# Performance work log

Hardware: AMD Instinct MI355X
Metric: run time of the kernel (lower is better)

Reference implementation:

```python
import jax, jax.numpy as jnp
import numpy as np

NUM_HOPS = 3

def _position_encoding(sentence_size, embedding_size):
    # Vectorized version of the double loop in the source.
    i = np.arange(1, embedding_size + 1, dtype=np.float32)[:, None]  # [E,1]
    j = np.arange(1, sentence_size + 1, dtype=np.float32)[None, :]   # [1,S]
    enc = (i - embedding_size / 2.0) * (j - sentence_size / 2.0)
    enc = 1.0 + 4.0 * enc / embedding_size / sentence_size
    return jnp.asarray(np.transpose(enc))  # [S, E]

def setup_inputs() -> dict:
    key = jax.random.key(0)
    ks = jax.random.split(key, 9)
    B, M, S, E, V, OUT = 16, 512, 32, 128, 32000, 128
    scale = 0.02
    return {
        "queries": jax.random.randint(ks[0], (B, S), 0, V, dtype=jnp.int32),
        "stories": jax.random.randint(ks[1], (B, M, S), 0, V, dtype=jnp.int32),
        "query_biases": jax.random.normal(ks[2], (V - 1, E), jnp.float32) * scale,
        "stories_biases": jax.random.normal(ks[3], (V - 1, E), jnp.float32) * scale,
        "memory_biases": jax.random.normal(ks[4], (M, E), jnp.float32) * scale,
        "output_biases": jax.random.normal(ks[5], (V - 1, E), jnp.float32) * scale,
        "w_intermediate": jax.random.normal(ks[6], (E, E), jnp.float32) * scale,
        "w_output": jax.random.normal(ks[7], (E, OUT), jnp.float32) * scale,
        "w_final": jax.random.normal(ks[8], (OUT, V), jnp.float32) * scale,
    }

def reference(queries, stories, query_biases, stories_biases, memory_biases,
              output_biases, w_intermediate, w_output, w_final):
    B, M, S = stories.shape
    E = query_biases.shape[1]
    enc = _position_encoding(S, E)  # [S, E]
    nil = jnp.zeros((1, E), dtype=query_biases.dtype)

    # Story memory: gather -> positional weight -> reduce over sentence axis.
    st_tab = jnp.concatenate([stories_biases, nil], axis=0)          # [V, E]
    mem_emb = st_tab[stories]                                        # [B,M,S,E]
    memory = jnp.einsum('bmse,se->bme', mem_emb, enc) + memory_biases

    # Query embedding.
    q_tab = jnp.concatenate([query_biases, nil], axis=0)
    q = jnp.einsum('bse,se->be', q_tab[queries], enc)                # [B,E]

    # Output memory.
    o_tab = jnp.concatenate([output_biases, nil], axis=0)
    output = jnp.einsum('bmse,se->bme', o_tab[stories], enc)         # [B,M,E]

    out_layer = q
    for hop in range(NUM_HOPS):
        probs = jax.nn.softmax(jnp.einsum('bme,be->bm', memory, q))  # [B,M]
        layer_out = jnp.einsum('bme,bm->be', output, probs)          # [B,E]
        w = w_output if hop == NUM_HOPS - 1 else w_intermediate
        out_layer = (q + layer_out) @ w
        q = out_layer                     # pre-nonlinearity state, as in source
        out_layer = jax.nn.relu(out_layer)

    return out_layer @ w_final            # [B, vocab]
```

## Files before the change

kernel.cpp:

```cpp
#include <hip/hip_runtime.h>

constexpr int kB  = 16;
constexpr int kM  = 512;
constexpr int kS  = 32;
constexpr int kE  = 128;
constexpr int kV  = 32000;
constexpr int kVN = kV - 1;
constexpr int kMS = 132;

__global__ __launch_bounds__(256) void embed_stories_kernel(
    const int*   __restrict__ stories,
    const float* __restrict__ st_bias,
    const float* __restrict__ out_bias,
    const float* __restrict__ mem_bias,
    float*       __restrict__ memory,
    float*       __restrict__ output,
    unsigned*    __restrict__ bar)
{
    __shared__ int sidx[2][kS];
    __shared__ __align__(16) float pm[8][kE];
    __shared__ __align__(16) float po[8][kE];

    const int t    = threadIdx.x;
    const int row0 = blockIdx.x * 2;
    if (t < 64) sidx[t >> 5][t & 31] = stories[row0 * kS + t];
    if (blockIdx.x == 0 && t < kB) bar[t] = 0u;
    __syncthreads();

    const int g    = t >> 5;
    const int lane = t & 31;
    const int p    = g >> 2;
    const int ph   = g & 3;
    const int e0   = lane * 4;
    const float ef0 = (float)(e0 - 63), ef1 = (float)(e0 - 62);
    const float ef2 = (float)(e0 - 61), ef3 = (float)(e0 - 60);

    float4 am = {0.f, 0.f, 0.f, 0.f};
    float4 ao = {0.f, 0.f, 0.f, 0.f};
    #pragma unroll
    for (int j = 0; j < 8; ++j) {
        const int s   = ph * 8 + j;
        const int idx = sidx[p][s];
        const int ci  = idx < kVN ? idx : (kVN - 1);
        const float live = (idx < kVN) ? 1.0f : 0.0f;
        const float sf = (float)(s - 15) * (1.0f / 1024.0f);
        const float4 vm = *(const float4*)(st_bias  + (size_t)ci * kE + e0);
        const float4 vo = *(const float4*)(out_bias + (size_t)ci * kE + e0);
        const float c0 = fmaf(ef0, sf, 1.0f) * live;
        const float c1 = fmaf(ef1, sf, 1.0f) * live;
        const float c2 = fmaf(ef2, sf, 1.0f) * live;
        const float c3 = fmaf(ef3, sf, 1.0f) * live;
        am.x = fmaf(vm.x, c0, am.x); am.y = fmaf(vm.y, c1, am.y);
        am.z = fmaf(vm.z, c2, am.z); am.w = fmaf(vm.w, c3, am.w);
        ao.x = fmaf(vo.x, c0, ao.x); ao.y = fmaf(vo.y, c1, ao.y);
        ao.z = fmaf(vo.z, c2, ao.z); ao.w = fmaf(vo.w, c3, ao.w);
    }
    *(float4*)&pm[g][e0] = am;
    *(float4*)&po[g][e0] = ao;
    __syncthreads();

    const int pr = t >> 7;
    const int e  = t & 127;
    const int row = row0 + pr;
    const int m   = row & (kM - 1);
    const float sm = pm[pr * 4 + 0][e] + pm[pr * 4 + 1][e] +
                     pm[pr * 4 + 2][e] + pm[pr * 4 + 3][e];
    const float so = po[pr * 4 + 0][e] + po[pr * 4 + 1][e] +
                     po[pr * 4 + 2][e] + po[pr * 4 + 3][e];
    memory[(size_t)row * kE + e] = sm + mem_bias[m * kE + e];
    output[(size_t)row * kE + e] = so;
}

__device__ __forceinline__ void group_barrier(unsigned* ctr, unsigned target)
{
    __syncthreads();
    if (threadIdx.x == 0) {
        __hip_atomic_fetch_add(ctr, 1u, __ATOMIC_RELEASE, __HIP_MEMORY_SCOPE_AGENT);
        while (__hip_atomic_load(ctr, __ATOMIC_RELAXED, __HIP_MEMORY_SCOPE_AGENT) < target)
            __builtin_amdgcn_s_sleep(2);
    }
    __syncthreads();
}
__device__ __forceinline__ void cstore(float* p, float v) {
    __hip_atomic_store(p, v, __ATOMIC_RELAXED, __HIP_MEMORY_SCOPE_AGENT);
}
__device__ __forceinline__ float cload(const float* p) {
    return __hip_atomic_load(p, __ATOMIC_RELAXED, __HIP_MEMORY_SCOPE_AGENT);
}

__global__ __launch_bounds__(1024) void hops_kernel(
    const int*   __restrict__ queries,
    const float* __restrict__ q_bias,
    const float* __restrict__ memory,
    const float* __restrict__ output,
    const float* __restrict__ w_int,
    const float* __restrict__ w_out,
    float*       __restrict__ numer,
    float*       __restrict__ denom,
    float*       __restrict__ xg,
    unsigned*    __restrict__ bar)
{
    __shared__ __align__(16) float mem_lds[128 * kMS];
    __shared__ __align__(16) float out_lds[128 * kE];
    __shared__ float sc_q[128];
    __shared__ __align__(16) float q_s[kE];
    __shared__ float xb[kE];
    __shared__ __align__(16) float part8[8][kE];
    __shared__ int qidx[kS];

    const int bid = blockIdx.x;
    const int b   = bid >> 2;
    const int qtr = bid & 3;
    const int t   = threadIdx.x;
    unsigned* ctr = bar + b;

    const float* memb = memory + ((size_t)b * kM + qtr * 128) * kE;
    const float* outb = output + ((size_t)b * kM + qtr * 128) * kE;
    #pragma unroll
    for (int i = 0; i < 4; ++i) {
        const int flat = t + i * 1024;
        const int rr = flat >> 5, ff = (flat & 31) * 4;
        *(float4*)&mem_lds[rr * kMS + ff] = *(const float4*)&memb[(size_t)rr * kE + ff];
        *(float4*)&out_lds[rr * kE  + ff] = *(const float4*)&outb[(size_t)rr * kE + ff];
    }
    if (t < kS) qidx[t] = queries[b * kS + t];
    __syncthreads();

    if (t < 256) {
        const int g = t >> 5, lane = t & 31, e0 = lane * 4;
        const float f0 = (float)(e0 - 63) * (1.0f / 1024.0f);
        const float f1 = (float)(e0 - 62) * (1.0f / 1024.0f);
        const float f2 = (float)(e0 - 61) * (1.0f / 1024.0f);
        const float f3 = (float)(e0 - 60) * (1.0f / 1024.0f);
        float4 a = {0.f, 0.f, 0.f, 0.f};
        #pragma unroll
        for (int j = 0; j < 4; ++j) {
            const int s   = g * 4 + j;
            const int idx = qidx[s];
            const int ci  = idx < kVN ? idx : (kVN - 1);
            const float live = (idx < kVN) ? 1.0f : 0.0f;
            const float sf = (float)(s - 15);
            const float4 v = *(const float4*)&q_bias[(size_t)ci * kE + e0];
            a.x = fmaf(v.x, fmaf(f0, sf, 1.f) * live, a.x);
            a.y = fmaf(v.y, fmaf(f1, sf, 1.f) * live, a.y);
            a.z = fmaf(v.z, fmaf(f2, sf, 1.f) * live, a.z);
            a.w = fmaf(v.w, fmaf(f3, sf, 1.f) * live, a.w);
        }
        *(float4*)&part8[g][e0] = a;
    }
    __syncthreads();
    if (t < kE) {
        float s = 0.f;
        #pragma unroll
        for (int g = 0; g < 8; ++g) s += part8[g][t];
        q_s[t] = s;
    }
    __syncthreads();

    const int grp = t >> 7;
    const int e   = t & 127;

    for (int hop = 0; hop < 3; ++hop) {
        {
            const int rw = t >> 3, sub = t & 7;
            const float4* qv = (const float4*)&q_s[sub * 16];
            const float4* mv = (const float4*)&mem_lds[rw * kMS + sub * 16];
            float d = 0.f;
            #pragma unroll
            for (int i = 0; i < 4; ++i) {
                const float4 m4 = mv[i], q4 = qv[i];
                d = fmaf(m4.x, q4.x, d); d = fmaf(m4.y, q4.y, d);
                d = fmaf(m4.z, q4.z, d); d = fmaf(m4.w, q4.w, d);
            }
            d += __shfl_down(d, 4);
            d += __shfl_down(d, 2);
            d += __shfl_down(d, 1);
            if (sub == 0) sc_q[rw] = __expf(d);
        }
        __syncthreads();

        {
            float acc = 0.f;
            const float* pp = &sc_q[grp * 16];
            const float* ob = &out_lds[grp * 16 * kE + e];
            #pragma unroll
            for (int j = 0; j < 16; ++j)
                acc = fmaf(pp[j], ob[j * kE], acc);
            part8[grp][e] = acc;
        }
        __syncthreads();

        const int pb = hop & 1;
        float* nq = numer + (((size_t)pb * kB + b) * 4 + qtr) * kE;
        if (t < kE) {
            float s = 0.f;
            #pragma unroll
            for (int g = 0; g < 8; ++g) s += part8[g][t];
            cstore(&nq[t], s);
        } else if (t < 192) {
            const int l = t - 128;
            float s2 = sc_q[l] + sc_q[l + 64];
            #pragma unroll
            for (int off = 32; off; off >>= 1) s2 += __shfl_down(s2, off);
            if (l == 0) cstore(&denom[((size_t)pb * kB + b) * 4 + qtr], s2);
        }

        group_barrier(ctr, 4u * (hop + 1));

        if (t < kE) {
            const float* nn = numer + ((size_t)pb * kB + b) * 4 * kE;
            const float* dd = denom + ((size_t)pb * kB + b) * 4;
            const float ns = cload(&nn[t]) + cload(&nn[kE + t]) +
                             cload(&nn[2 * kE + t]) + cload(&nn[3 * kE + t]);
            const float ds = cload(&dd[0]) + cload(&dd[1]) +
                             cload(&dd[2]) + cload(&dd[3]);
            xb[t] = q_s[t] + ns / ds;
        }
        __syncthreads();

        {
            const float* w = (hop == 2) ? w_out : w_int;
            float acc = 0.f;
            #pragma unroll
            for (int j = 0; j < 16; ++j) {
                const int k = grp * 16 + j;
                acc = fmaf(xb[k], w[k * kE + e], acc);
            }
            part8[grp][e] = acc;
        }
        __syncthreads();
        if (t < kE) {
            float s = 0.f;
            #pragma unroll
            for (int g = 0; g < 8; ++g) s += part8[g][t];
            q_s[t] = s;
        }
        __syncthreads();
    }

    if (qtr == 0 && t < kE) xg[t * kB + b] = fmaxf(q_s[t], 0.f);
}

__global__ __launch_bounds__(256) void final_kernel(
    const float* __restrict__ xg,
    const float* __restrict__ wf,
    float*       __restrict__ out)
{
    __shared__ float ps[128 * kB];
    const int t = threadIdx.x;
    const int v = blockIdx.x * 128 + (t & 127);
    const int h = t >> 7;

    float acc[kB];
    #pragma unroll
    for (int b = 0; b < kB; ++b) acc[b] = 0.f;

    const int e0 = h * 64;
    #pragma unroll 4
    for (int ei = 0; ei < 64; ++ei) {
        const int e = e0 + ei;
        const float wv = wf[(size_t)e * kV + v];
        const float* xr = xg + e * kB;
        #pragma unroll
        for (int b = 0; b < kB; ++b) acc[b] = fmaf(xr[b], wv, acc[b]);
    }
    if (h == 1) {
        #pragma unroll
        for (int b = 0; b < kB; ++b) ps[(t & 127) * kB + b] = acc[b];
    }
    __syncthreads();
    if (h == 0) {
        #pragma unroll
        for (int b = 0; b < kB; ++b)
            out[(size_t)b * kV + v] = acc[b] + ps[(t & 127) * kB + b];
    }
}

extern "C" void kernel_launch(void* const* d_in, const int* in_sizes, int n_in,
                              void* d_out, int out_size, void* d_ws, size_t ws_size,
                              hipStream_t stream)
{
    const int*   queries  = (const int*)  d_in[0];
    const int*   stories  = (const int*)  d_in[1];
    const float* q_bias   = (const float*)d_in[2];
    const float* st_bias  = (const float*)d_in[3];
    const float* mem_bias = (const float*)d_in[4];
    const float* out_bias = (const float*)d_in[5];
    const float* w_int    = (const float*)d_in[6];
    const float* w_out    = (const float*)d_in[7];
    const float* w_final  = (const float*)d_in[8];
    float* out = (float*)d_out;

    float* memory = (float*)d_ws;
    float* output = memory + (size_t)kB * kM * kE;
    float* numer  = output + (size_t)kB * kM * kE;
    float* denom  = numer  + 2 * kB * 4 * kE;
    float* xg     = denom  + 2 * kB * 4;
    unsigned* bar = (unsigned*)(xg + kE * kB);

    embed_stories_kernel<<<dim3((kB * kM) / 2), dim3(256), 0, stream>>>(
        stories, st_bias, out_bias, mem_bias, memory, output, bar);

    hops_kernel<<<dim3(64), dim3(1024), 0, stream>>>(
        queries, q_bias, memory, output, w_int, w_out,
        numer, denom, xg, bar);

    final_kernel<<<dim3(kV / 128), dim3(256), 0, stream>>>(xg, w_final, out);
}
```

Before: 166.4 us.

## Stage embedding gathers through LDS with global_load_lds in the story embed kernel

Rewrites the story embedding kernel to gather table rows directly into shared memory using the global_load_lds builtin. It processes the 32 sentence positions in four chunks of eight, with a barrier after each load and after each compute pass. Each thread then accumulates one embedding element per table for two rows, which replaces the earlier float4 register gather and cross-group reduction. The intent is to raise load efficiency and drop the reduction step, at the cost of extra syncthreads and serialized load/compute phases with no double buffering.

```diff
diff --git a/kernel.cpp b/kernel.cpp
--- a/kernel.cpp
+++ b/kernel.cpp
@@ -18,57 +18,63 @@
     unsigned*    __restrict__ bar)
 {
     __shared__ int sidx[2][kS];
-    __shared__ __align__(16) float pm[8][kE];
-    __shared__ __align__(16) float po[8][kE];
-
-    const int t    = threadIdx.x;
+    __shared__ __align__(16) float stage[16 * 256];
+
+    const int t = threadIdx.x;
+    if (t < 64) sidx[t >> 5][t & 31] = stories[blockIdx.x * 2 * kS + t];
+    if (blockIdx.x == 0 && t < kB) bar[t] = 0u;
+    __syncthreads();
+
+    const int wave = t >> 6;
+    const int lane = t & 63;
+    const int half = lane >> 5;
+    const int l16  = lane & 31;
+
+    const int tab = t >> 7;
+    const int e   = t & 127;
+    const float ef = (float)(e - 63) * (1.0f / 1024.0f);
+    float acc0 = 0.f, acc1 = 0.f;
+
+    for (int c = 0; c < 4; ++c) {
+        #pragma unroll
+        for (int k = 0; k < 4; ++k) {
+            const int idx4 = wave * 4 + k;
+            const int sl   = idx4 >> 1;
+            const int tb   = idx4 & 1;
+            const int s    = c * 8 + sl;
+            const int widx = sidx[half][s];
+            const int ci   = widx < kVN ? widx : (kVN - 1);
+            const float* g = (tb ? out_bias : st_bias)
+                             + (size_t)ci * kE + l16 * 4;
+            float* lb = &stage[(sl * 2 + tb) * 256];
+            __builtin_amdgcn_global_load_lds(
+                (const __attribute__((address_space(1))) void*)g,
+                (__attribute__((address_space(3))) void*)lb, 16, 0, 0);
+        }
+        __syncthreads();
+
+        #pragma unroll
+        for (int sl = 0; sl < 8; ++sl) {
+            const int s = c * 8 + sl;
+            const float enc = fmaf(ef, (float)(s - 15), 1.0f);
+            const float l0 = (sidx[0][s] < kVN) ? enc : 0.f;
+            const float l1 = (sidx[1][s] < kVN) ? enc : 0.f;
+            const float* sp = &stage[(sl * 2 + tab) * 256];
+            acc0 = fmaf(sp[e],       l0, acc0);
+            acc1 = fmaf(sp[128 + e], l1, acc1);
+        }
+        __syncthreads();
+    }
+
     const int row0 = blockIdx.x * 2;
-    if (t < 64) sidx[t >> 5][t & 31] = stories[row0 * kS + t];
-    if (blockIdx.x == 0 && t < kB) bar[t] = 0u;
-    __syncthreads();
-
-    const int g    = t >> 5;
-    const int lane = t & 31;
-    const int p    = g >> 2;
-    const int ph   = g & 3;
-    const int e0   = lane * 4;
-    const float ef0 = (float)(e0 - 63), ef1 = (float)(e0 - 62);
-    const float ef2 = (float)(e0 - 61), ef3 = (float)(e0 - 60);
-
-    float4 am = {0.f, 0.f, 0.f, 0.f};
-    float4 ao = {0.f, 0.f, 0.f, 0.f};
-    #pragma unroll
-    for (int j = 0; j < 8; ++j) {
-        const int s   = ph * 8 + j;
-        const int idx = sidx[p][s];
-        const int ci  = idx < kVN ? idx : (kVN - 1);
-        const float live = (idx < kVN) ? 1.0f : 0.0f;
-        const float sf = (float)(s - 15) * (1.0f / 1024.0f);
-        const float4 vm = *(const float4*)(st_bias  + (size_t)ci * kE + e0);
-        const float4 vo = *(const float4*)(out_bias + (size_t)ci * kE + e0);
-        const float c0 = fmaf(ef0, sf, 1.0f) * live;
-        const float c1 = fmaf(ef1, sf, 1.0f) * live;
-        const float c2 = fmaf(ef2, sf, 1.0f) * live;
-        const float c3 = fmaf(ef3, sf, 1.0f) * live;
-        am.x = fmaf(vm.x, c0, am.x); am.y = fmaf(vm.y, c1, am.y);
-        am.z = fmaf(vm.z, c2, am.z); am.w = fmaf(vm.w, c3, am.w);
-        ao.x = fmaf(vo.x, c0, ao.x); ao.y = fmaf(vo.y, c1, ao.y);
-        ao.z = fmaf(vo.z, c2, ao.z); ao.w = fmaf(vo.w, c3, ao.w);
-    }
-    *(float4*)&pm[g][e0] = am;
-    *(float4*)&po[g][e0] = ao;
-    __syncthreads();
-
-    const int pr = t >> 7;
-    const int e  = t & 127;
-    const int row = row0 + pr;
-    const int m   = row & (kM - 1);
-    const float sm = pm[pr * 4 + 0][e] + pm[pr * 4 + 1][e] +
-                     pm[pr * 4 + 2][e] + pm[pr * 4 + 3][e];
-    const float so = po[pr * 4 + 0][e] + po[pr * 4 + 1][e] +
-                     po[pr * 4 + 2][e] + po[pr * 4 + 3][e];
-    memory[(size_t)row * kE + e] = sm + mem_bias[m * kE + e];
-    output[(size_t)row * kE + e] = so;
+    if (tab == 0) {
+        const int m0 = row0 & (kM - 1);
+        memory[(size_t)row0 * kE + e]       = acc0 + mem_bias[m0 * kE + e];
+        memory[(size_t)(row0 + 1) * kE + e] = acc1 + mem_bias[(m0 + 1) * kE + e];
+    } else {
+        output[(size_t)row0 * kE + e]       = acc0;
+        output[(size_t)(row0 + 1) * kE + e] = acc1;
+    }
 }
 
 __device__ __forceinline__ void group_barrier(unsigned* ctr, unsigned target)
```

New measurement: 167.1 us. No clear change (+0.5%).

## Fuse final vocab projection into hops kernel via grid-wide spin barrier

Applied to the files above, without the earlier changes.

Merges the final_kernel into the hops kernel. A global spin barrier across all 64 blocks makes each block wait for the relu'd hop result, after which it projects onto 500 vocab columns using the LDS it already has. This removes one kernel launch and the gap between launches. In exchange the 16MB w_final read now runs on only 64 blocks instead of 250, which lowers memory-level parallelism for that bandwidth-bound stage.

```diff
diff --git a/kernel.cpp b/kernel.cpp
--- a/kernel.cpp
+++ b/kernel.cpp
@@ -24,7 +24,7 @@
     const int t    = threadIdx.x;
     const int row0 = blockIdx.x * 2;
     if (t < 64) sidx[t >> 5][t & 31] = stories[row0 * kS + t];
-    if (blockIdx.x == 0 && t < kB) bar[t] = 0u;
+    if (blockIdx.x == 0 && t < 32) bar[t] = 0u;
     __syncthreads();
 
     const int g    = t >> 5;
@@ -71,7 +71,7 @@
     output[(size_t)row * kE + e] = so;
 }
 
-__device__ __forceinline__ void group_barrier(unsigned* ctr, unsigned target)
+__device__ __forceinline__ void spin_barrier(unsigned* ctr, unsigned target)
 {
     __syncthreads();
     if (threadIdx.x == 0) {
@@ -88,17 +88,19 @@
     return __hip_atomic_load(p, __ATOMIC_RELAXED, __HIP_MEMORY_SCOPE_AGENT);
 }
 
-__global__ __launch_bounds__(1024) void hops_kernel(
+__global__ __launch_bounds__(1024) void hops_final_kernel(
     const int*   __restrict__ queries,
     const float* __restrict__ q_bias,
     const float* __restrict__ memory,
     const float* __restrict__ output,
     const float* __restrict__ w_int,
     const float* __restrict__ w_out,
+    const float* __restrict__ w_final,
     float*       __restrict__ numer,
     float*       __restrict__ denom,
     float*       __restrict__ xg,
-    unsigned*    __restrict__ bar)
+    unsigned*    __restrict__ bar,
+    float*       __restrict__ out)
 {
     __shared__ __align__(16) float mem_lds[128 * kMS];
     __shared__ __align__(16) float out_lds[128 * kE];
@@ -205,7 +207,7 @@
             if (l == 0) cstore(&denom[((size_t)pb * kB + b) * 4 + qtr], s2);
         }
 
-        group_barrier(ctr, 4u * (hop + 1));
+        spin_barrier(ctr, 4u * (hop + 1));
 
         if (t < kE) {
             const float* nn = numer + ((size_t)pb * kB + b) * 4 * kE;
@@ -238,41 +240,42 @@
         __syncthreads();
     }
 
-    if (qtr == 0 && t < kE) xg[t * kB + b] = fmaxf(q_s[t], 0.f);
-}
-
-__global__ __launch_bounds__(256) void final_kernel(
-    const float* __restrict__ xg,
-    const float* __restrict__ wf,
-    float*       __restrict__ out)
-{
-    __shared__ float ps[128 * kB];
-    const int t = threadIdx.x;
-    const int v = blockIdx.x * 128 + (t & 127);
-    const int h = t >> 7;
-
+    if (qtr == 0 && t < kE) cstore(&xg[t * kB + b], fmaxf(q_s[t], 0.f));
+    spin_barrier(bar + 16, 64u);
+
+    float* xs = mem_lds;
+    float* ps = out_lds;
+    xs[t]        = cload(&xg[t]);
+    xs[t + 1024] = cload(&xg[t + 1024]);
+    __syncthreads();
+
+    const int h = t >> 9;
+    const int c = t & 511;
+    const bool valid = c < 500;
+    const int v = bid * 500 + c;
     float acc[kB];
     #pragma unroll
-    for (int b = 0; b < kB; ++b) acc[b] = 0.f;
-
-    const int e0 = h * 64;
-    #pragma unroll 4
-    for (int ei = 0; ei < 64; ++ei) {
-        const int e = e0 + ei;
-        const float wv = wf[(size_t)e * kV + v];
-        const float* xr = xg + e * kB;
+    for (int bb = 0; bb < kB; ++bb) acc[bb] = 0.f;
+    if (valid) {
+        const int e0 = h * 64;
+        #pragma unroll 4
+        for (int ei = 0; ei < 64; ++ei) {
+            const int ee = e0 + ei;
+            const float wv = w_final[(size_t)ee * kV + v];
+            const float* xr = xs + ee * kB;
+            #pragma unroll
+            for (int bb = 0; bb < kB; ++bb) acc[bb] = fmaf(xr[bb], wv, acc[bb]);
+        }
+        if (h == 1) {
+            #pragma unroll
+            for (int bb = 0; bb < kB; ++bb) ps[c * kB + bb] = acc[bb];
+        }
+    }
+    __syncthreads();
+    if (valid && h == 0) {
         #pragma unroll
-        for (int b = 0; b < kB; ++b) acc[b] = fmaf(xr[b], wv, acc[b]);
-    }
-    if (h == 1) {
-        #pragma unroll
-        for (int b = 0; b < kB; ++b) ps[(t & 127) * kB + b] = acc[b];
-    }
-    __syncthreads();
-    if (h == 0) {
-        #pragma unroll
-        for (int b = 0; b < kB; ++b)
-            out[(size_t)b * kV + v] = acc[b] + ps[(t & 127) * kB + b];
+        for (int bb = 0; bb < kB; ++bb)
+            out[(size_t)bb * kV + v] = acc[bb] + ps[c * kB + bb];
     }
 }
 
@@ -301,9 +304,7 @@
     embed_stories_kernel<<<dim3((kB * kM) / 2), dim3(256), 0, stream>>>(
         stories, st_bias, out_bias, mem_bias, memory, output, bar);
 
-    hops_kernel<<<dim3(64), dim3(1024), 0, stream>>>(
-        queries, q_bias, memory, output, w_int, w_out,
-        numer, denom, xg, bar);
-
-    final_kernel<<<dim3(kV / 128), dim3(256), 0, stream>>>(xg, w_final, out);
-}
+    hops_final_kernel<<<dim3(64), dim3(1024), 0, stream>>>(
+        queries, q_bias, memory, output, w_int, w_out, w_final,
+        numer, denom, xg, bar, out);
+}
```

After: 168.0 us. Within noise of the previous version (+1.0%).
